# Kernel tuning notes

Measured on AMD Instinct MI355X. Metric: run time of the kernel, lower is better.

## Reference

```python
import jax, jax.numpy as jnp
import numpy as np

B, CH, TD, H, DH = 64, 512, 256, 4, 64
T_LAT, T_TXT = 1000, 512
SCALE = TD ** -0.5  # note: module scales by text_dim**-0.5, not head_dim**-0.5


def setup_inputs() -> dict:
    key = jax.random.key(0)
    ks = jax.random.split(key, 12)
    half = DH // 2
    theta = (1.0 / (10000.0 ** (jnp.arange(half, dtype=jnp.float32) / half))).reshape(1, 1, half) * 10.0
    increments = jnp.arange(1000, dtype=jnp.float32).reshape(1, 1000, 1)
    return {
        "x": jax.random.normal(ks[0], (B, CH, T_LAT), jnp.float32),
        "text_emb": jax.random.normal(ks[1], (B, TD, T_TXT), jnp.float32),
        "latent_mask": jnp.ones((B, 1, T_LAT), jnp.float32),
        "text_mask": jax.random.randint(ks[2], (B, 1, T_TXT), 0, 2, jnp.int32),
        "Wq": jax.random.normal(ks[3], (TD, CH), jnp.float32) * 0.02,
        "bq": jax.random.normal(ks[4], (TD,), jnp.float32) * 0.02,
        "Wk": jax.random.normal(ks[5], (TD, TD), jnp.float32) * 0.02,
        "bk": jax.random.normal(ks[6], (TD,), jnp.float32) * 0.02,
        "Wv": jax.random.normal(ks[7], (TD, TD), jnp.float32) * 0.02,
        "bv": jax.random.normal(ks[8], (TD,), jnp.float32) * 0.02,
        "Wo": jax.random.normal(ks[9], (CH, TD), jnp.float32) * 0.02,
        "bo": jax.random.normal(ks[10], (CH,), jnp.float32) * 0.02,
        "theta": theta,
        "increments": increments,
    }


def _rope(x, seq_len, theta, increments):
    # x: (B, H, S, D); angles built from normalized positions * theta
    half = x.shape[-1] // 2
    pos = increments[:, :seq_len, :] / seq_len          # (1, S, 1)
    ang = (pos * theta)[:, None]                        # (1, 1, S, half)
    x1, x2 = x[..., :half], x[..., half:]
    c, s = jnp.cos(ang), jnp.sin(ang)
    return jnp.concatenate([x1 * c - x2 * s, x1 * s + x2 * c], axis=-1)


def reference(x, text_emb, latent_mask, text_mask, Wq, bq, Wk, bk, Wv, bv, Wo, bo, theta, increments):
    b, _, t_lat = x.shape
    t_txt = text_emb.shape[2]
    # projections: inputs are channel-first, project the transposed (B, T, C)
    q = jnp.einsum('bct,dc->btd', x, Wq) + bq           # (B, T_lat, TD)
    k = jnp.einsum('bct,dc->btd', text_emb, Wk) + bk    # (B, T_txt, TD)
    v = jnp.einsum('bct,dc->btd', text_emb, Wv) + bv
    # split heads -> (B, H, T, DH)
    q = q.reshape(b, t_lat, H, DH).transpose(0, 2, 1, 3)
    k = k.reshape(b, t_txt, H, DH).transpose(0, 2, 1, 3)
    v = v.reshape(b, t_txt, H, DH).transpose(0, 2, 1, 3)
    q = _rope(q, t_lat, theta, increments)
    k = _rope(k, t_txt, theta, increments)
    attn = jnp.einsum('bhqd,bhkd->bhqk', q, k) * SCALE  # (B, H, T_lat, T_txt)
    mask = text_mask[:, None]                           # (B, 1, 1, T_txt) broadcast
    attn = jnp.where(mask == 0, -jnp.inf, attn)
    attn = jax.nn.softmax(attn, axis=-1)
    out = jnp.einsum('bhqk,bhkd->bhqd', attn, v)        # (B, H, T_lat, DH)
    out = out.transpose(0, 2, 1, 3).reshape(b, t_lat, TD)
    out = jnp.einsum('btd,cd->bct', out, Wo) + bo[None, :, None]  # (B, CH, T_lat)
    out = x + out
    out = out * latent_mask
    return out
```

## Files before the change

### kernel.cpp

```cpp
#include <hip/hip_runtime.h>
#include <hip/hip_bf16.h>

typedef __hip_bfloat16 bf16;
typedef __attribute__((ext_vector_type(8))) short short8;
typedef __attribute__((ext_vector_type(4))) float float4v;

#define B_    64
#define CH_   512
#define TD_   256
#define H_    4
#define DH_   64
#define TLAT  1000
#define TTXT  512
#define SCALE_ 0.0625f

__device__ __forceinline__ float cvt(float x) { return x; }
__device__ __forceinline__ float cvt(bf16 x)  { return __bfloat162float(x); }
__device__ __forceinline__ void stv(float* p, float v) { *p = v; }
__device__ __forceinline__ void stv(bf16* p, float v)  { *p = __float2bfloat16(v); }

__device__ __forceinline__ unsigned short f2bu(float f) {
  bf16 h = __float2bfloat16(f);
  unsigned short u; __builtin_memcpy(&u, &h, 2); return u;
}
__device__ __forceinline__ float bu2f(unsigned short u) {
  bf16 h; __builtin_memcpy(&h, &u, 2); return __bfloat162float(h);
}

__device__ __forceinline__ int swz(int row, int col) {
  return col ^ ((row & 7) << 3);
}

__device__ __forceinline__ float4 ld4(const float* p) { return *(const float4*)p; }
__device__ __forceinline__ float4 ld4(const bf16* p) {
  ushort4 u = *(const ushort4*)p;
  return make_float4(bu2f(u.x), bu2f(u.y), bu2f(u.z), bu2f(u.w));
}
__device__ __forceinline__ void st4(float* p, float4 v) { *(float4*)p = v; }
__device__ __forceinline__ void st4(bf16* p, float4 v) {
  ushort4 u = make_ushort4(f2bu(v.x), f2bu(v.y), f2bu(v.z), f2bu(v.w));
  *(ushort4*)p = u;
}

__global__ void detect_k(const void* inc, int* flag) {
  const float* f = (const float*)inc;
  float err = fabsf(f[1] - 1.f) + fabsf(f[2] - 2.f) + fabsf(f[3] - 3.f);
  *flag = (err < 0.5f) ? 0 : 1;
}

template<typename T>
__device__ __forceinline__ void cvtw_body(const void* a, const void* b2,
                                          const void* c, const void* d,
                                          unsigned short* out) {
  int i = blockIdx.x * 256 + threadIdx.x;
  float v;
  if (i < 131072)      v = cvt(((const T*)a)[i]);
  else if (i < 196608) v = cvt(((const T*)b2)[i - 131072]);
  else if (i < 262144) v = cvt(((const T*)c)[i - 196608]);
  else                 v = cvt(((const T*)d)[i - 262144]);
  out[i] = f2bu(v);
}

__global__ __launch_bounds__(256) void cvtw_k(
    const int* __restrict__ flag, const void* a, const void* b2,
    const void* c, const void* d, unsigned short* out) {
  if (*flag) cvtw_body<bf16>(a, b2, c, d, out);
  else       cvtw_body<float>(a, b2, c, d, out);
}

template<typename T>
__device__ __forceinline__ void transpose_body(
    const void* inv, size_t ioff, size_t strideIn,
    unsigned short* out, size_t strideOut, int K, int M,
    unsigned int (*Ls)[33]) {
  const T* in = (const T*)inv + ioff + (size_t)blockIdx.z * strideIn;
  unsigned short* ob = out + (size_t)blockIdx.z * strideOut;
  const int m0 = blockIdx.x * 64, k0 = blockIdx.y * 64;
  const int tid = threadIdx.x;
  const int ml = tid & 63;
  int mrd = m0 + ml; if (mrd >= M) mrd = M - 1;
#pragma unroll
  for (int it = 0; it < 8; it++) {
    int kp = it * 4 + (tid >> 6);
    int k = k0 + kp * 2;
    float v0 = cvt(in[(size_t)k * M + mrd]);
    float v1 = cvt(in[(size_t)(k + 1) * M + mrd]);
    Ls[ml][kp] = (unsigned)f2bu(v0) | ((unsigned)f2bu(v1) << 16);
  }
  __syncthreads();
#pragma unroll
  for (int it = 0; it < 8; it++) {
    int idx = it * 256 + tid;
    int my = idx >> 5, kk = idx & 31;
    int m = m0 + my;
    if (m < M)
      *(unsigned*)&ob[(size_t)m * K + k0 + kk * 2] = Ls[my][kk];
  }
}

__global__ __launch_bounds__(256) void transpose_k(
    const int* __restrict__ flag, const void* in, size_t ioff, size_t strideIn,
    unsigned short* out, size_t strideOut, int K, int M) {
  __shared__ unsigned int Ls[64][33];
  if (*flag) transpose_body<bf16>(in, ioff, strideIn, out, strideOut, K, M, Ls);
  else       transpose_body<float>(in, ioff, strideIn, out, strideOut, K, M, Ls);
}

__device__ __forceinline__ void gemm_core(
    const unsigned short* __restrict__ Ab, int lda, int M,
    const unsigned short* __restrict__ Bb, int ldb, int N, int K,
    int m0, int n0,
    unsigned short (*As)[40], unsigned short (*Bs)[40],
    float4v (&acc)[4][4]) {
  const int tid = threadIdx.x;
  const int lane = tid & 63, w = tid >> 6;
  const int lq = lane & 15, quad = lane >> 4;
  const int wm = (w >> 1) * 64, wn = (w & 1) * 64;
  const int srow = tid >> 2;
  const int sch  = (tid & 3) * 8;

#pragma unroll
  for (int i = 0; i < 4; i++)
#pragma unroll
    for (int j = 0; j < 4; j++) acc[i][j] = (float4v){0.f, 0.f, 0.f, 0.f};

  for (int k0 = 0; k0 < K; k0 += 32) {
    uint4 va[2], vb[2];
#pragma unroll
    for (int hf = 0; hf < 2; hf++) {
      int ra = m0 + hf * 64 + srow; ra = (ra < M) ? ra : (M - 1);
      int rb = n0 + hf * 64 + srow; rb = (rb < N) ? rb : (N - 1);
      va[hf] = *(const uint4*)(Ab + (size_t)ra * lda + k0 + sch);
      vb[hf] = *(const uint4*)(Bb + (size_t)rb * ldb + k0 + sch);
    }
    __syncthreads();
#pragma unroll
    for (int hf = 0; hf < 2; hf++) {
      *(uint4*)&As[hf * 64 + srow][sch] = va[hf];
      *(uint4*)&Bs[hf * 64 + srow][sch] = vb[hf];
    }
    __syncthreads();
    short8 af[4], bfr[4];
#pragma unroll
    for (int i = 0; i < 4; i++) {
      af[i]  = *(const short8*)&As[wm + i * 16 + lq][quad * 8];
      bfr[i] = *(const short8*)&Bs[wn + i * 16 + lq][quad * 8];
    }
#pragma unroll
    for (int i = 0; i < 4; i++)
#pragma unroll
      for (int j = 0; j < 4; j++)
        acc[i][j] = __builtin_amdgcn_mfma_f32_16x16x32_bf16(af[i], bfr[j], acc[i][j], 0, 0, 0);
  }
}

template<typename T>
__device__ __forceinline__ void epi_store(
    float4v (&acc)[4][4], int m0, int n0, unsigned short* Cb, int ldc, int M, int N,
    const void* biasv, int biasByM, unsigned short* scr) {
  const T* bias = (const T*)biasv;
  const int tid = threadIdx.x;
  const int lane = tid & 63, w = tid >> 6;
  const int lq = lane & 15, quad = lane >> 4;
  const int wm = (w >> 1) * 64, wn = (w & 1) * 64;
  const int rbase = (w >> 1) * 16 + quad * 4;
  const int lr = tid >> 3, ck = tid & 7;
  const int mbase = m0 + (lr >> 4) * 64 + (lr & 15);
#pragma unroll
  for (int i = 0; i < 4; i++) {
    __syncthreads();
#pragma unroll
    for (int j = 0; j < 4; j++) {
      float bn_ = biasByM ? 0.f : cvt(bias[n0 + wn + j * 16 + lq]);
#pragma unroll
      for (int r = 0; r < 4; r++) {
        float bb = biasByM ? cvt(bias[m0 + wm + i * 16 + quad * 4 + r]) : bn_;
        scr[(rbase + r) * 136 + wn + j * 16 + lq] = f2bu(acc[i][j][r] + bb);
      }
    }
    __syncthreads();
    int m = mbase + i * 16;
    if (m < M) {
#pragma unroll
      for (int u = 0; u < 2; u++) {
        int c = u * 64 + ck * 8;
        *(uint4*)&Cb[(size_t)m * ldc + n0 + c] = *(const uint4*)&scr[lr * 136 + c];
      }
    }
  }
}

__global__ __launch_bounds__(256) void gemm_bf(
    const int* __restrict__ flag,
    const unsigned short* __restrict__ A, size_t strideA, int lda, int M,
    const unsigned short* __restrict__ B, size_t strideB, int ldb, int N, int K,
    unsigned short* C, size_t strideC, int ldc,
    const void* bias, int biasByM) {
  __shared__ __align__(16) unsigned char smem[20480];
  unsigned short (*As)[40] = (unsigned short (*)[40])smem;
  unsigned short (*Bs)[40] = (unsigned short (*)[40])(smem + 10240);
  const int bz = blockIdx.z;
  const int m0 = blockIdx.x * 128, n0 = blockIdx.y * 128;
  float4v acc[4][4];
  gemm_core(A + (size_t)bz * strideA, lda, M,
            B + (size_t)bz * strideB, ldb, N, K, m0, n0, As, Bs, acc);
  unsigned short* Cb = C + (size_t)bz * strideC;
  unsigned short* scr = (unsigned short*)smem;
  if (*flag) epi_store<bf16>(acc, m0, n0, Cb, ldc, M, N, bias, biasByM, scr);
  else       epi_store<float>(acc, m0, n0, Cb, ldc, M, N, bias, biasByM, scr);
}

template<typename T>
__device__ __forceinline__ void epi_out(
    float4v (&acc)[4][4], int m0, int n0, int bz, int M, int N,
    const void* biasv, const void* Xv, size_t xoffE,
    const void* lmv, size_t lmoffE, void* Outv, size_t ooffE, size_t strideO,
    float* scr) {
  const T* bias = (const T*)biasv;
  const T* X  = (const T*)Xv + xoffE;
  const T* lm = (const T*)lmv + lmoffE;
  T* Out      = (T*)Outv + ooffE;
  const int tid = threadIdx.x;
  const int lane = tid & 63, w = tid >> 6;
  const int lq = lane & 15, quad = lane >> 4;
  const int wm = (w >> 1) * 64, wn = (w & 1) * 64;
  const int rbase = (w >> 1) * 16 + quad * 4;
  const int col = (lane & 31) * 4;
  const int rw  = w * 2 + (lane >> 5);
#pragma unroll
  for (int i = 0; i < 4; i++) {
    __syncthreads();
#pragma unroll
    for (int j = 0; j < 4; j++) {
#pragma unroll
      for (int r = 0; r < 4; r++) {
        int m = m0 + wm + i * 16 + quad * 4 + r;
        scr[(rbase + r) * 136 + wn + j * 16 + lq] = acc[i][j][r] + cvt(bias[m]);
      }
    }
    __syncthreads();
#pragma unroll
    for (int p = 0; p < 4; p++) {
      int lr2 = p * 8 + rw;
      int m = m0 + (lr2 >> 4) * 64 + (lr2 & 15) + i * 16;
      int n = n0 + col;
      if (m < M && n < N) {
        size_t rowo = (size_t)bz * strideO + (size_t)m * TLAT;
        float4 sv = *(const float4*)&scr[lr2 * 136 + col];
        float4 vx = ld4(X + rowo + n);
        float4 vl = ld4(lm + (size_t)bz * TLAT + n);
        float4 v;
        v.x = (sv.x + vx.x) * vl.x;
        v.y = (sv.y + vx.y) * vl.y;
        v.z = (sv.z + vx.z) * vl.z;
        v.w = (sv.w + vx.w) * vl.w;
        st4(Out + rowo + n, v);
      }
    }
  }
}

__global__ __launch_bounds__(256) void gemm_bf_out(
    const int* __restrict__ flag,
    const unsigned short* __restrict__ A, size_t strideA, int lda, int M,
    const unsigned short* __restrict__ B, size_t strideB, int ldb, int N, int K,
    const void* bias, const void* X, size_t xoffE,
    const void* lmask, size_t lmoffE, void* Out, size_t ooffE, size_t strideO) {
  __shared__ __align__(16) unsigned char smem[20480];
  unsigned short (*As)[40] = (unsigned short (*)[40])smem;
  unsigned short (*Bs)[40] = (unsigned short (*)[40])(smem + 10240);

  int bx = blockIdx.x, by = blockIdx.y, bz = blockIdx.z;
  if (gridDim.x == 4 && gridDim.y == 8 && gridDim.z == 64) {
    int lin = blockIdx.x + (blockIdx.y << 2) + (blockIdx.z << 5);
    int k = lin & 7, j = lin >> 3;
    by = j & 7; bx = (j >> 3) & 3; bz = (j >> 5) | (k << 3);
  }
  const int m0 = bx * 128, n0 = by * 128;

  float4v acc[4][4];
  gemm_core(A + (size_t)bz * strideA, lda, M,
            B + (size_t)bz * strideB, ldb, N, K, m0, n0, As, Bs, acc);
  float* scr = (float*)smem;
  if (*flag) epi_out<bf16>(acc, m0, n0, bz, M, N, bias, X, xoffE, lmask, lmoffE, Out, ooffE, strideO, scr);
  else       epi_out<float>(acc, m0, n0, bz, M, N, bias, X, xoffE, lmask, lmoffE, Out, ooffE, strideO, scr);
}

template<typename T>
__device__ __forceinline__ void rope_body(
    unsigned short* buf, const void* incv, const void* thetav,
    int T_, float inv_seq, int total) {
  const T* inc = (const T*)incv;
  const T* theta = (const T*)thetav;
  int gid = blockIdx.x * 256 + threadIdx.x;
  if (gid >= total) return;
  int jb = gid & 3;
  int h  = (gid >> 2) & 3;
  int t  = (gid >> 4) % T_;
  int b  = gid / (T_ * 16);
  float ab = cvt(inc[t]) * inv_seq;
  size_t base = (size_t)(b * T_ + t) * TD_ + h * 64 + jb * 8;
  short8 v1 = *(const short8*)&buf[base];
  short8 v2 = *(const short8*)&buf[base + 32];
  short8 r1, r2;
#pragma unroll
  for (int e = 0; e < 8; e++) {
    float ang = ab * cvt(theta[jb * 8 + e]);
    float s, c;
    __sincosf(ang, &s, &c);
    float x1 = bu2f((unsigned short)v1[e]);
    float x2 = bu2f((unsigned short)v2[e]);
    r1[e] = (short)f2bu(x1 * c - x2 * s);
    r2[e] = (short)f2bu(x1 * s + x2 * c);
  }
  *(short8*)&buf[base]      = r1;
  *(short8*)&buf[base + 32] = r2;
}

__global__ __launch_bounds__(256) void rope_k(
    const int* __restrict__ flag, unsigned short* buf, const void* inc,
    const void* theta, int T_, float inv_seq, int total) {
  if (*flag) rope_body<bf16>(buf, inc, theta, T_, inv_seq, total);
  else       rope_body<float>(buf, inc, theta, T_, inv_seq, total);
}

__global__ __launch_bounds__(256) void attn_mfma(
    const unsigned short* __restrict__ Q, const unsigned short* __restrict__ K,
    const unsigned short* __restrict__ Vt, const int* __restrict__ tmask,
    unsigned short* __restrict__ AO) {
  const int b = blockIdx.z, h = blockIdx.y, q0 = blockIdx.x * 64;
  __shared__ unsigned short Ks[128][64];
  __shared__ unsigned short Vs[64][128];
  __shared__ unsigned short Ps[4][16][128];
  __shared__ float maskf[TTXT];

  const int tid = threadIdx.x;
  const int w = tid >> 6, lane = tid & 63;
  const int lq = lane & 15, quad = lane >> 4;

  short8 qa0 = (short8){0, 0, 0, 0, 0, 0, 0, 0};
  short8 qa1 = (short8){0, 0, 0, 0, 0, 0, 0, 0};
  {
    int qrow = q0 + w * 16 + lq;
    if (qrow < TLAT) {
      const unsigned short* qp = Q + ((size_t)(b * TLAT + qrow) * TD_ + h * 64);
      qa0 = *(const short8*)(qp + quad * 8);
      qa1 = *(const short8*)(qp + 32 + quad * 8);
    }
  }
  maskf[tid]       = (float)tmask[b * TTXT + tid];
  maskf[tid + 256] = (float)tmask[b * TTXT + 256 + tid];

  float m_old[4] = {-1e30f, -1e30f, -1e30f, -1e30f};
  float l[4] = {0.f, 0.f, 0.f, 0.f};
  float4v Oacc[4];
#pragma unroll
  for (int i = 0; i < 4; i++) Oacc[i] = (float4v){0.f, 0.f, 0.f, 0.f};

  for (int kt = 0; kt < 4; kt++) {
    __syncthreads();
#pragma unroll
    for (int it = 0; it < 4; it++) {
      int c = it * 256 + tid;
      int row = c >> 3, col = (c & 7) * 8;
      *(uint4*)&Ks[row][swz(row, col)] =
        *(const uint4*)(K + ((size_t)(b * TTXT + kt * 128 + row) * TD_ + h * 64 + col));
    }
#pragma unroll
    for (int it = 0; it < 4; it++) {
      int c = it * 256 + tid;
      int row = c >> 4, col = (c & 15) * 8;
      *(uint4*)&Vs[row][swz(row, col)] =
        *(const uint4*)(Vt + (((size_t)b * TD_ + h * 64 + row) * TTXT + kt * 128 + col));
    }
    __syncthreads();

    float4v Sacc[8];
#pragma unroll
    for (int nt = 0; nt < 8; nt++) {
      int krow = nt * 16 + lq;
      short8 kb0 = *(const short8*)&Ks[krow][swz(krow, quad * 8)];
      short8 kb1 = *(const short8*)&Ks[krow][swz(krow, 32 + quad * 8)];
      float4v s = (float4v){0.f, 0.f, 0.f, 0.f};
      s = __builtin_amdgcn_mfma_f32_16x16x32_bf16(qa0, kb0, s, 0, 0, 0);
      s = __builtin_amdgcn_mfma_f32_16x16x32_bf16(qa1, kb1, s, 0, 0, 0);
      Sacc[nt] = s;
    }
    float mk[8];
#pragma unroll
    for (int nt = 0; nt < 8; nt++) mk[nt] = maskf[kt * 128 + nt * 16 + lq];

#pragma unroll
    for (int nt = 0; nt < 8; nt++)
#pragma unroll
      for (int r = 0; r < 4; r++) {
        float sv = Sacc[nt][r] * SCALE_;
        Sacc[nt][r] = (mk[nt] != 0.f) ? sv : -1e30f;
      }

#pragma unroll
    for (int r = 0; r < 4; r++) {
      float mx = -1e30f;
#pragma unroll
      for (int nt = 0; nt < 8; nt++) mx = fmaxf(mx, Sacc[nt][r]);
      mx = fmaxf(mx, __shfl_xor(mx, 1));
      mx = fmaxf(mx, __shfl_xor(mx, 2));
      mx = fmaxf(mx, __shfl_xor(mx, 4));
      mx = fmaxf(mx, __shfl_xor(mx, 8));
      float mnew = fmaxf(m_old[r], mx);
      float alpha = __expf(m_old[r] - mnew);
      float ps = 0.f;
      int prow = quad * 4 + r;
#pragma unroll
      for (int nt = 0; nt < 8; nt++) {
        float p = (mk[nt] != 0.f) ? __expf(Sacc[nt][r] - mnew) : 0.f;
        ps += p;
        Ps[w][prow][swz(prow, nt * 16 + lq)] = f2bu(p);
      }
      ps += __shfl_xor(ps, 1);
      ps += __shfl_xor(ps, 2);
      ps += __shfl_xor(ps, 4);
      ps += __shfl_xor(ps, 8);
      l[r] = alpha * l[r] + ps;
      m_old[r] = mnew;
#pragma unroll
      for (int dt = 0; dt < 4; dt++) Oacc[dt][r] *= alpha;
    }

#pragma unroll
    for (int dt = 0; dt < 4; dt++) {
#pragma unroll
      for (int ks = 0; ks < 4; ks++) {
        short8 pa = *(const short8*)&Ps[w][lq][swz(lq, ks * 32 + quad * 8)];
        int vrow = dt * 16 + lq;
        short8 vb = *(const short8*)&Vs[vrow][swz(vrow, ks * 32 + quad * 8)];
        Oacc[dt] = __builtin_amdgcn_mfma_f32_16x16x32_bf16(pa, vb, Oacc[dt], 0, 0, 0);
      }
    }
  }

#pragma unroll
  for (int r = 0; r < 4; r++) {
    int q = q0 + w * 16 + quad * 4 + r;
    if (q < TLAT) {
      float linv = 1.0f / fmaxf(l[r], 1e-30f);
#pragma unroll
      for (int dt = 0; dt < 4; dt++) {
        int d = h * 64 + dt * 16 + lq;
        AO[(size_t)(b * TLAT + q) * TD_ + d] = f2bu(Oacc[dt][r] * linv);
      }
    }
  }
}

extern "C" void kernel_launch(void* const* d_in, const int* in_sizes, int n_in,
                              void* d_out, int out_size, void* d_ws, size_t ws_size,
                              hipStream_t stream) {
  const void* x        = d_in[0];
  const void* text_emb = d_in[1];
  const void* lmask    = d_in[2];
  const int*  tmask    = (const int*)d_in[3];
  const void* Wq = d_in[4];
  const void* bq = d_in[5];
  const void* Wk = d_in[6];
  const void* bk = d_in[7];
  const void* Wv = d_in[8];
  const void* bv = d_in[9];
  const void* Wo = d_in[10];
  const void* bo = d_in[11];
  const void* theta = d_in[12];
  const void* inc   = d_in[13];

  int* dflag = (int*)d_ws;
  unsigned short* wbuf = (unsigned short*)((char*)d_ws + 256);
  unsigned short* scratch = wbuf + 393216;
  size_t used = 256 + (size_t)393216 * 2;
  size_t avail = (ws_size > used) ? ws_size - used : 0;

  const size_t per_b_elems = 512000 + 131072 + 256000 + 131072 + 131072 + 256000;
  const size_t per_b_bytes = per_b_elems * 2;
  int Bc = (int)(avail / per_b_bytes);
  if (Bc > B_) Bc = B_;
  if (Bc < 1) Bc = 1;

  unsigned short* xT   = scratch;
  unsigned short* embT = xT   + (size_t)Bc * 512000;
  unsigned short* qb   = embT + (size_t)Bc * 131072;
  unsigned short* kb   = qb   + (size_t)Bc * 256000;
  unsigned short* vtb  = kb   + (size_t)Bc * 131072;
  unsigned short* aob  = vtb  + (size_t)Bc * 131072;

  detect_k<<<1, 1, 0, stream>>>(inc, dflag);
  cvtw_k<<<1536, 256, 0, stream>>>(dflag, Wq, Wk, Wv, Wo, wbuf);
  const unsigned short* Wqb = wbuf;
  const unsigned short* Wkb = wbuf + 131072;
  const unsigned short* Wvb = wbuf + 196608;
  const unsigned short* Wob = wbuf + 262144;

  for (int b0 = 0; b0 < B_; b0 += Bc) {
    int bn = B_ - b0; if (bn > Bc) bn = Bc;
    size_t xoffE = (size_t)b0 * CH_ * TLAT;
    size_t eoffE = (size_t)b0 * TD_ * TTXT;

    transpose_k<<<dim3(16, 8, bn), 256, 0, stream>>>(dflag, x, xoffE, 512000,
                                                     xT, 512000, CH_, TLAT);
    transpose_k<<<dim3(8, 4, bn), 256, 0, stream>>>(dflag, text_emb, eoffE, 131072,
                                                    embT, 131072, TD_, TTXT);

    gemm_bf<<<dim3(8, 2, bn), 256, 0, stream>>>(dflag, xT, 512000, 512, TLAT,
                                                Wqb, 0, 512, TD_, CH_,
                                                qb, 256000, TD_, bq, 0);
    gemm_bf<<<dim3(4, 2, bn), 256, 0, stream>>>(dflag, embT, 131072, 256, TTXT,
                                                Wkb, 0, 256, TD_, TD_,
                                                kb, 131072, TD_, bk, 0);
    gemm_bf<<<dim3(2, 4, bn), 256, 0, stream>>>(dflag, Wvb, 0, 256, TD_,
                                                embT, 131072, 256, TTXT, TD_,
                                                vtb, 131072, TTXT, bv, 1);

    int totq = bn * TLAT * 16;
    rope_k<<<(totq + 255) / 256, 256, 0, stream>>>(dflag, qb, inc, theta, TLAT, 1.0f / TLAT, totq);
    int totk = bn * TTXT * 16;
    rope_k<<<(totk + 255) / 256, 256, 0, stream>>>(dflag, kb, inc, theta, TTXT, 1.0f / TTXT, totk);

    attn_mfma<<<dim3(16, H_, bn), 256, 0, stream>>>(qb, kb, vtb,
                                                    tmask + (size_t)b0 * TTXT, aob);

    gemm_bf_out<<<dim3(4, 8, bn), 256, 0, stream>>>(dflag, Wob, 0, 256, CH_,
                                                    aob, 256000, 256, TLAT, TD_,
                                                    bo, x, xoffE,
                                                    lmask, (size_t)b0 * TLAT,
                                                    d_out, xoffE, (size_t)CH_ * TLAT);
  }
}
```

Measured before the change: 701.1 us.

## Fuse RoPE into Q/K projection epilogue and prefetch GEMM/epilogue global loads

Removes the separate rope_k kernels by applying the rotary embedding in the Q and K projection GEMM epilogue. Each 64-wide head is paired with columns j and j+2 within the warp's 64-column slice. This saves two extra read-modify-write passes over the q and k buffers, plus two launches per batch chunk. It also adds register double-buffering of the next K-slice global loads in gemm_core, and prefetches the residual X rows in the output epilogue, to overlap loads with MFMA and store work. The cost is more registers, and correctness relies on each warp's 64-column slice lining up with one head.

```diff
diff --git a/kernel.cpp b/kernel.cpp
--- a/kernel.cpp
+++ b/kernel.cpp
@@ -119,20 +119,26 @@
   const int srow = tid >> 2;
   const int sch  = (tid & 3) * 8;
 
+  int ra[2], rb[2];
+#pragma unroll
+  for (int hf = 0; hf < 2; hf++) {
+    int r0 = m0 + hf * 64 + srow; ra[hf] = (r0 < M) ? r0 : (M - 1);
+    int r1 = n0 + hf * 64 + srow; rb[hf] = (r1 < N) ? r1 : (N - 1);
+  }
+
 #pragma unroll
   for (int i = 0; i < 4; i++)
 #pragma unroll
     for (int j = 0; j < 4; j++) acc[i][j] = (float4v){0.f, 0.f, 0.f, 0.f};
 
+  uint4 va[2], vb[2];
+#pragma unroll
+  for (int hf = 0; hf < 2; hf++) {
+    va[hf] = *(const uint4*)(Ab + (size_t)ra[hf] * lda + sch);
+    vb[hf] = *(const uint4*)(Bb + (size_t)rb[hf] * ldb + sch);
+  }
+
   for (int k0 = 0; k0 < K; k0 += 32) {
-    uint4 va[2], vb[2];
-#pragma unroll
-    for (int hf = 0; hf < 2; hf++) {
-      int ra = m0 + hf * 64 + srow; ra = (ra < M) ? ra : (M - 1);
-      int rb = n0 + hf * 64 + srow; rb = (rb < N) ? rb : (N - 1);
-      va[hf] = *(const uint4*)(Ab + (size_t)ra * lda + k0 + sch);
-      vb[hf] = *(const uint4*)(Bb + (size_t)rb * ldb + k0 + sch);
-    }
     __syncthreads();
 #pragma unroll
     for (int hf = 0; hf < 2; hf++) {
@@ -140,6 +146,16 @@
       *(uint4*)&Bs[hf * 64 + srow][sch] = vb[hf];
     }
     __syncthreads();
+
+    uint4 na[2] = {va[0], va[1]}, nb[2] = {vb[0], vb[1]};
+    if (k0 + 32 < K) {
+#pragma unroll
+      for (int hf = 0; hf < 2; hf++) {
+        na[hf] = *(const uint4*)(Ab + (size_t)ra[hf] * lda + k0 + 32 + sch);
+        nb[hf] = *(const uint4*)(Bb + (size_t)rb[hf] * ldb + k0 + 32 + sch);
+      }
+    }
+
     short8 af[4], bfr[4];
 #pragma unroll
     for (int i = 0; i < 4; i++) {
@@ -151,14 +167,19 @@
 #pragma unroll
       for (int j = 0; j < 4; j++)
         acc[i][j] = __builtin_amdgcn_mfma_f32_16x16x32_bf16(af[i], bfr[j], acc[i][j], 0, 0, 0);
+
+    va[0] = na[0]; va[1] = na[1]; vb[0] = nb[0]; vb[1] = nb[1];
   }
 }
 
 template<typename T>
 __device__ __forceinline__ void epi_store(
     float4v (&acc)[4][4], int m0, int n0, unsigned short* Cb, int ldc, int M, int N,
-    const void* biasv, int biasByM, unsigned short* scr) {
+    const void* biasv, int biasByM, unsigned short* scr,
+    const void* incv, const void* thetav, float inv_seq, int ropeT) {
   const T* bias = (const T*)biasv;
+  const T* inc_ = (const T*)incv;
+  const T* theta_ = (const T*)thetav;
   const int tid = threadIdx.x;
   const int lane = tid & 63, w = tid >> 6;
   const int lq = lane & 15, quad = lane >> 4;
@@ -169,13 +190,34 @@
 #pragma unroll
   for (int i = 0; i < 4; i++) {
     __syncthreads();
-#pragma unroll
-    for (int j = 0; j < 4; j++) {
-      float bn_ = biasByM ? 0.f : cvt(bias[n0 + wn + j * 16 + lq]);
-#pragma unroll
-      for (int r = 0; r < 4; r++) {
-        float bb = biasByM ? cvt(bias[m0 + wm + i * 16 + quad * 4 + r]) : bn_;
-        scr[(rbase + r) * 136 + wn + j * 16 + lq] = f2bu(acc[i][j][r] + bb);
+    if (ropeT > 0) {
+#pragma unroll
+      for (int jlo = 0; jlo < 2; jlo++) {
+        float b1 = cvt(bias[n0 + wn + jlo * 16 + lq]);
+        float b2 = cvt(bias[n0 + wn + (jlo + 2) * 16 + lq]);
+        float th = cvt(theta_[jlo * 16 + lq]);
+#pragma unroll
+        for (int r = 0; r < 4; r++) {
+          int t = m0 + wm + i * 16 + quad * 4 + r;
+          int tt = (t < ropeT) ? t : (ropeT - 1);
+          float ang = cvt(inc_[tt]) * inv_seq * th;
+          float s, c;
+          __sincosf(ang, &s, &c);
+          float v1 = acc[i][jlo][r] + b1;
+          float v2 = acc[i][jlo + 2][r] + b2;
+          scr[(rbase + r) * 136 + wn + jlo * 16 + lq]       = f2bu(v1 * c - v2 * s);
+          scr[(rbase + r) * 136 + wn + (jlo + 2) * 16 + lq] = f2bu(v1 * s + v2 * c);
+        }
+      }
+    } else {
+#pragma unroll
+      for (int j = 0; j < 4; j++) {
+        float bn_ = biasByM ? 0.f : cvt(bias[n0 + wn + j * 16 + lq]);
+#pragma unroll
+        for (int r = 0; r < 4; r++) {
+          float bb = biasByM ? cvt(bias[m0 + wm + i * 16 + quad * 4 + r]) : bn_;
+          scr[(rbase + r) * 136 + wn + j * 16 + lq] = f2bu(acc[i][j][r] + bb);
+        }
       }
     }
     __syncthreads();
@@ -195,7 +237,8 @@
     const unsigned short* __restrict__ A, size_t strideA, int lda, int M,
     const unsigned short* __restrict__ B, size_t strideB, int ldb, int N, int K,
     unsigned short* C, size_t strideC, int ldc,
-    const void* bias, int biasByM) {
+    const void* bias, int biasByM,
+    const void* inc, const void* theta, float inv_seq, int ropeT) {
   __shared__ __align__(16) unsigned char smem[20480];
   unsigned short (*As)[40] = (unsigned short (*)[40])smem;
   unsigned short (*Bs)[40] = (unsigned short (*)[40])(smem + 10240);
@@ -206,8 +249,8 @@
             B + (size_t)bz * strideB, ldb, N, K, m0, n0, As, Bs, acc);
   unsigned short* Cb = C + (size_t)bz * strideC;
   unsigned short* scr = (unsigned short*)smem;
-  if (*flag) epi_store<bf16>(acc, m0, n0, Cb, ldc, M, N, bias, biasByM, scr);
-  else       epi_store<float>(acc, m0, n0, Cb, ldc, M, N, bias, biasByM, scr);
+  if (*flag) epi_store<bf16>(acc, m0, n0, Cb, ldc, M, N, bias, biasByM, scr, inc, theta, inv_seq, ropeT);
+  else       epi_store<float>(acc, m0, n0, Cb, ldc, M, N, bias, biasByM, scr, inc, theta, inv_seq, ropeT);
 }
 
 template<typename T>
@@ -227,36 +270,59 @@
   const int rbase = (w >> 1) * 16 + quad * 4;
   const int col = (lane & 31) * 4;
   const int rw  = w * 2 + (lane >> 5);
+  const int n = n0 + col;
+  const bool nok = (n < N);
+  float4 vl = make_float4(0.f, 0.f, 0.f, 0.f);
+  if (nok) vl = ld4(lm + (size_t)bz * TLAT + n);
+
+  float4 px[4];
+#pragma unroll
+  for (int p = 0; p < 4; p++) {
+    int lr2 = p * 8 + rw;
+    int m = m0 + (lr2 >> 4) * 64 + (lr2 & 15);
+    px[p] = (m < M && nok) ? ld4(X + (size_t)bz * strideO + (size_t)m * TLAT + n)
+                           : make_float4(0.f, 0.f, 0.f, 0.f);
+  }
 #pragma unroll
   for (int i = 0; i < 4; i++) {
     __syncthreads();
 #pragma unroll
-    for (int j = 0; j < 4; j++) {
+    for (int j = 0; j < 4; j++)
 #pragma unroll
       for (int r = 0; r < 4; r++) {
         int m = m0 + wm + i * 16 + quad * 4 + r;
         scr[(rbase + r) * 136 + wn + j * 16 + lq] = acc[i][j][r] + cvt(bias[m]);
       }
-    }
-    __syncthreads();
+    __syncthreads();
+    float4 nx[4];
+#pragma unroll
+    for (int p = 0; p < 4; p++) nx[p] = px[p];
+    if (i < 3) {
+#pragma unroll
+      for (int p = 0; p < 4; p++) {
+        int lr2 = p * 8 + rw;
+        int m = m0 + (lr2 >> 4) * 64 + (lr2 & 15) + (i + 1) * 16;
+        nx[p] = (m < M && nok) ? ld4(X + (size_t)bz * strideO + (size_t)m * TLAT + n)
+                               : make_float4(0.f, 0.f, 0.f, 0.f);
+      }
+    }
 #pragma unroll
     for (int p = 0; p < 4; p++) {
       int lr2 = p * 8 + rw;
       int m = m0 + (lr2 >> 4) * 64 + (lr2 & 15) + i * 16;
-      int n = n0 + col;
-      if (m < M && n < N) {
+      if (m < M && nok) {
         size_t rowo = (size_t)bz * strideO + (size_t)m * TLAT;
         float4 sv = *(const float4*)&scr[lr2 * 136 + col];
-        float4 vx = ld4(X + rowo + n);
-        float4 vl = ld4(lm + (size_t)bz * TLAT + n);
         float4 v;
-        v.x = (sv.x + vx.x) * vl.x;
-        v.y = (sv.y + vx.y) * vl.y;
-        v.z = (sv.z + vx.z) * vl.z;
-        v.w = (sv.w + vx.w) * vl.w;
+        v.x = (sv.x + px[p].x) * vl.x;
+        v.y = (sv.y + px[p].y) * vl.y;
+        v.z = (sv.z + px[p].z) * vl.z;
+        v.w = (sv.w + px[p].w) * vl.w;
         st4(Out + rowo + n, v);
       }
     }
+#pragma unroll
+    for (int p = 0; p < 4; p++) px[p] = nx[p];
   }
 }
 
@@ -284,44 +350,6 @@
   float* scr = (float*)smem;
   if (*flag) epi_out<bf16>(acc, m0, n0, bz, M, N, bias, X, xoffE, lmask, lmoffE, Out, ooffE, strideO, scr);
   else       epi_out<float>(acc, m0, n0, bz, M, N, bias, X, xoffE, lmask, lmoffE, Out, ooffE, strideO, scr);
-}
-
-template<typename T>
-__device__ __forceinline__ void rope_body(
-    unsigned short* buf, const void* incv, const void* thetav,
-    int T_, float inv_seq, int total) {
-  const T* inc = (const T*)incv;
-  const T* theta = (const T*)thetav;
-  int gid = blockIdx.x * 256 + threadIdx.x;
-  if (gid >= total) return;
-  int jb = gid & 3;
-  int h  = (gid >> 2) & 3;
-  int t  = (gid >> 4) % T_;
-  int b  = gid / (T_ * 16);
-  float ab = cvt(inc[t]) * inv_seq;
-  size_t base = (size_t)(b * T_ + t) * TD_ + h * 64 + jb * 8;
-  short8 v1 = *(const short8*)&buf[base];
-  short8 v2 = *(const short8*)&buf[base + 32];
-  short8 r1, r2;
-#pragma unroll
-  for (int e = 0; e < 8; e++) {
-    float ang = ab * cvt(theta[jb * 8 + e]);
-    float s, c;
-    __sincosf(ang, &s, &c);
-    float x1 = bu2f((unsigned short)v1[e]);
-    float x2 = bu2f((unsigned short)v2[e]);
-    r1[e] = (short)f2bu(x1 * c - x2 * s);
-    r2[e] = (short)f2bu(x1 * s + x2 * c);
-  }
-  *(short8*)&buf[base]      = r1;
-  *(short8*)&buf[base + 32] = r2;
-}
-
-__global__ __launch_bounds__(256) void rope_k(
-    const int* __restrict__ flag, unsigned short* buf, const void* inc,
-    const void* theta, int T_, float inv_seq, int total) {
-  if (*flag) rope_body<bf16>(buf, inc, theta, T_, inv_seq, total);
-  else       rope_body<float>(buf, inc, theta, T_, inv_seq, total);
 }
 
 __global__ __launch_bounds__(256) void attn_mfma(
@@ -509,18 +537,16 @@
 
     gemm_bf<<<dim3(8, 2, bn), 256, 0, stream>>>(dflag, xT, 512000, 512, TLAT,
                                                 Wqb, 0, 512, TD_, CH_,
-                                                qb, 256000, TD_, bq, 0);
+                                                qb, 256000, TD_, bq, 0,
+                                                inc, theta, 1.0f / TLAT, TLAT);
     gemm_bf<<<dim3(4, 2, bn), 256, 0, stream>>>(dflag, embT, 131072, 256, TTXT,
                                                 Wkb, 0, 256, TD_, TD_,
-                                                kb, 131072, TD_, bk, 0);
+                                                kb, 131072, TD_, bk, 0,
+                                                inc, theta, 1.0f / TTXT, TTXT);
     gemm_bf<<<dim3(2, 4, bn), 256, 0, stream>>>(dflag, Wvb, 0, 256, TD_,
                                                 embT, 131072, 256, TTXT, TD_,
-                                                vtb, 131072, TTXT, bv, 1);
-
-    int totq = bn * TLAT * 16;
-    rope_k<<<(totq + 255) / 256, 256, 0, stream>>>(dflag, qb, inc, theta, TLAT, 1.0f / TLAT, totq);
-    int totk = bn * TTXT * 16;
-    rope_k<<<(totk + 255) / 256, 256, 0, stream>>>(dflag, kb, inc, theta, TTXT, 1.0f / TTXT, totk);
+                                                vtb, 131072, TTXT, bv, 1,
+                                                inc, theta, 0.f, 0);
 
     attn_mfma<<<dim3(16, H_, bn), 256, 0, stream>>>(qb, kb, vtb,
                                                     tmask + (size_t)b0 * TTXT, aob);
```

New measurement: 945.7 us. +34.9%, slower.
